# Performance work log

Measured on AMD Instinct MI355X. Metric: run time of the kernel, lower is better.

The kernel has to match this reference:

```python
import jax, jax.numpy as jnp
import numpy as np

N_NODES = 100000
N_EDGES = 600000
VOCAB = 50000
EMBED_DIM = 128
HIDDEN_DIM = 128


def gcn_conv(h, W, b, src, dst, n_nodes):
    """PyG GCNConv: x' = D^{-1/2} (A+I) D^{-1/2} X W + b.
    src/dst already include self-loops."""
    hw = h @ W                                   # [N, out]
    deg = jnp.zeros((n_nodes,), hw.dtype).at[dst].add(1.0)   # in-degree incl. self-loop
    dinv = jax.lax.rsqrt(deg)                    # deg >= 1 thanks to self-loops
    norm = dinv[src] * dinv[dst]                 # [E+N]
    msgs = norm[:, None] * hw[src]               # gather [E+N, out]
    out = jnp.zeros_like(hw).at[dst].add(msgs)   # scatter-aggregate
    return out + b


def setup_inputs() -> dict:
    key = jax.random.key(0)
    ks = jax.random.split(key, 8)
    x = jax.random.randint(ks[0], (N_NODES,), 0, VOCAB, dtype=jnp.int64 if jax.config.jax_enable_x64 else jnp.int32)
    edge_index = jax.random.randint(ks[1], (2, N_EDGES), 0, N_NODES, dtype=jnp.int32)
    emb = jax.random.normal(ks[2], (VOCAB, EMBED_DIM), dtype=jnp.float32)
    # Glorot-style scale for GCN weights
    W1 = jax.random.normal(ks[3], (EMBED_DIM, HIDDEN_DIM), dtype=jnp.float32) * (1.0 / np.sqrt(EMBED_DIM))
    b1 = jnp.zeros((HIDDEN_DIM,), dtype=jnp.float32)
    W2 = jax.random.normal(ks[4], (HIDDEN_DIM, HIDDEN_DIM), dtype=jnp.float32) * (1.0 / np.sqrt(HIDDEN_DIM))
    b2 = jnp.zeros((HIDDEN_DIM,), dtype=jnp.float32)
    return {"x": x, "edge_index": edge_index, "emb": emb, "W1": W1, "b1": b1, "W2": W2, "b2": b2}


def reference(x, edge_index, emb, W1, b1, W2, b2):
    n = x.shape[0]
    loops = jnp.arange(n, dtype=edge_index.dtype)
    src = jnp.concatenate([edge_index[0], loops])  # add self-loops once
    dst = jnp.concatenate([edge_index[1], loops])
    h = emb[x]                                     # [N, embed_dim] embedding lookup
    h = jax.nn.relu(gcn_conv(h, W1, b1, src, dst, n))
    h = jax.nn.relu(gcn_conv(h, W2, b2, src, dst, n))
    return h
```

## Files before the change

### kernel.cpp

```cpp
#include <hip/hip_runtime.h>


#define NDIM 128
#define PAD_K 136
#define SCAN_IPT 4
#define SCAN_BLK 256
#define SCAN_IPB (SCAN_BLK * SCAN_IPT)

typedef __bf16 bf16x8 __attribute__((ext_vector_type(8)));
typedef float f32x4 __attribute__((ext_vector_type(4)));

__device__ __forceinline__ float bf2f(unsigned short u) {
    union { unsigned int i; float f; } c;
    c.i = (unsigned int)u << 16;
    return c.f;
}
__device__ __forceinline__ unsigned short f2bf(float f) {
    __bf16 b = (__bf16)f;
    return __builtin_bit_cast(unsigned short, b);
}
__device__ __forceinline__ void unpack8(uint4 q, float* f) {
    f[0] = bf2f((unsigned short)(q.x & 0xffff));
    f[1] = bf2f((unsigned short)(q.x >> 16));
    f[2] = bf2f((unsigned short)(q.y & 0xffff));
    f[3] = bf2f((unsigned short)(q.y >> 16));
    f[4] = bf2f((unsigned short)(q.z & 0xffff));
    f[5] = bf2f((unsigned short)(q.z >> 16));
    f[6] = bf2f((unsigned short)(q.w & 0xffff));
    f[7] = bf2f((unsigned short)(q.w >> 16));
}

__global__ void degree_count(const int* __restrict__ dst, int* __restrict__ cnt, int E) {
    int e = blockIdx.x * blockDim.x + threadIdx.x;
    if (e < E) atomicAdd(&cnt[dst[e]], 1);
}

__global__ void scan_blocks(const int* __restrict__ in, int* __restrict__ out,
                            int* __restrict__ bsums, int n) {
    __shared__ int lds[SCAN_BLK];
    const int t = threadIdx.x;
    const int base = blockIdx.x * SCAN_IPB + t * SCAN_IPT;
    int v[SCAN_IPT];
    int s = 0;
#pragma unroll
    for (int k = 0; k < SCAN_IPT; ++k) { v[k] = (base + k < n) ? in[base + k] : 0; s += v[k]; }
    lds[t] = s;
    __syncthreads();
    for (int off = 1; off < SCAN_BLK; off <<= 1) {
        int x = (t >= off) ? lds[t - off] : 0;
        __syncthreads();
        lds[t] += x;
        __syncthreads();
    }
    if (t == SCAN_BLK - 1) bsums[blockIdx.x] = lds[t];
    int run = (t == 0) ? 0 : lds[t - 1];
#pragma unroll
    for (int k = 0; k < SCAN_IPT; ++k) {
        if (base + k < n) out[base + k] = run;
        run += v[k];
    }
}

__global__ void scan_partials(int* __restrict__ bsums, int nb) {
    __shared__ int lds[128];
    const int t = threadIdx.x;
    lds[t] = (t < nb) ? bsums[t] : 0;
    __syncthreads();
    for (int off = 1; off < 128; off <<= 1) {
        int x = (t >= off) ? lds[t - off] : 0;
        __syncthreads();
        lds[t] += x;
        __syncthreads();
    }
    if (t < nb) bsums[t] = (t == 0) ? 0 : lds[t - 1];
}

__global__ void add_offsets_dinv_wt(int* __restrict__ rp, const int* __restrict__ bsums,
                                    const int* __restrict__ cnt, float* __restrict__ dinv, int n,
                                    int nblkA,
                                    const float* __restrict__ W1, const float* __restrict__ W2,
                                    unsigned short* __restrict__ WT1,
                                    unsigned short* __restrict__ WT2) {
    if ((int)blockIdx.x < nblkA) {
        int i = blockIdx.x * blockDim.x + threadIdx.x;
        if (i < n) {
            rp[i] += bsums[i / SCAN_IPB];
            dinv[i] = rsqrtf((float)cnt[i] + 1.0f);
        }
    } else {
        int c = (blockIdx.x - nblkA) * blockDim.x + threadIdx.x;
        int cc = c & 16383;
        int j = cc >> 7, k = cc & 127;
        if (c < 16384) WT1[cc] = f2bf(W1[k * 128 + j]);
        else if (c < 32768) WT2[cc] = f2bf(W2[k * 128 + j]);
    }
}

__global__ void fill_edges(const int* __restrict__ src, const int* __restrict__ dst,
                           int* __restrict__ rp, const int* __restrict__ x,
                           const float* __restrict__ dinv, int4* __restrict__ ew, int E) {
    const int stride = gridDim.x * blockDim.x;
    int e = blockIdx.x * blockDim.x + threadIdx.x;
#pragma unroll
    for (int k = 0; k < 2; ++k, e += stride) {
        if (e < E) {
            int d = dst[e], s = src[e];
            int xs = x[s];
            float ds = dinv[s];
            int p = atomicAdd(&rp[d], 1);
            ew[p] = make_int4(s, xs, __float_as_int(ds), 0);
        }
    }
}

template <int MODE, bool SCALE>
__global__ __launch_bounds__(256, 4)
void gemm_mfma(const void* __restrict__ Asrc, const unsigned short* __restrict__ WTb,
               const float* __restrict__ dinv, unsigned short* __restrict__ outb, int n) {
    __shared__ __bf16 sBT[128 * PAD_K];
    const int tid = threadIdx.x;
    const int rbase = blockIdx.x * 64;

    {
        const uint4* bsrc = (const uint4*)WTb;
#pragma unroll
        for (int i = 0; i < 8; ++i) {
            int c = tid + i * 256;
            int j = c >> 4, u = c & 15;
            *(uint4*)&sBT[j * PAD_K + u * 8] = bsrc[c];
        }
    }
    __syncthreads();

    const int wave = tid >> 6, lane = tid & 63;
    const int quad = lane >> 4, lrow = lane & 15;
    int arow = rbase + wave * 16 + lrow;
    if (arow >= n) arow = n - 1;

    f32x4 acc[8];
#pragma unroll
    for (int nt = 0; nt < 8; ++nt) acc[nt] = (f32x4)0.0f;

#pragma unroll
    for (int ks = 0; ks < 4; ++ks) {
        const int kb = ks * 32 + quad * 8;
        bf16x8 a;
        if (MODE == 0) {
            const float4* A4 = (const float4*)Asrc;
            float4 v0 = A4[(size_t)arow * 32 + (kb >> 2)];
            float4 v1 = A4[(size_t)arow * 32 + (kb >> 2) + 1];
            a = (bf16x8){(__bf16)v0.x, (__bf16)v0.y, (__bf16)v0.z, (__bf16)v0.w,
                         (__bf16)v1.x, (__bf16)v1.y, (__bf16)v1.z, (__bf16)v1.w};
        } else {
            a = *(const bf16x8*)((const unsigned short*)Asrc + (size_t)arow * 128 + kb);
        }
#pragma unroll
        for (int nt = 0; nt < 8; ++nt) {
            bf16x8 b = *(const bf16x8*)&sBT[(nt * 16 + lrow) * PAD_K + kb];
            acc[nt] = __builtin_amdgcn_mfma_f32_16x16x32_bf16(a, b, acc[nt], 0, 0, 0);
        }
    }

#pragma unroll
    for (int r = 0; r < 4; ++r) {
        int grow = rbase + wave * 16 + quad * 4 + r;
        if (grow < n) {
            float dsc = SCALE ? dinv[grow] : 1.0f;
            unsigned short* orow = outb + (size_t)grow * NDIM + lrow;
#pragma unroll
            for (int nt = 0; nt < 8; ++nt)
                orow[nt * 16] = f2bf(SCALE ? dsc * acc[nt][r] : acc[nt][r]);
        }
    }
}

__global__ void aggregate1(const unsigned short* __restrict__ tab, const int* __restrict__ x,
                           const int* __restrict__ rp, const int4* __restrict__ ew,
                           const float* __restrict__ dinv, const float* __restrict__ bias,
                           unsigned short* __restrict__ outb, int n) {
    int t = blockIdx.x * blockDim.x + threadIdx.x;
    int i = t >> 4, u = t & 15;
    if (i >= n) return;
    const uint4* tab4 = (const uint4*)tab;
    float di = dinv[i];
    float acc[8];
    {
        float f[8];
        unpack8(tab4[(size_t)x[i] * 16 + u], f);
#pragma unroll
        for (int k = 0; k < 8; ++k) acc[k] = di * f[k];
    }
    int j = (i == 0) ? 0 : rp[i - 1];
    const int end = rp[i];
    for (; j + 4 <= end; j += 4) {
        int4 e0 = ew[j], e1 = ew[j + 1], e2 = ew[j + 2], e3 = ew[j + 3];
        uint4 q0 = tab4[(size_t)e0.y * 16 + u];
        uint4 q1 = tab4[(size_t)e1.y * 16 + u];
        uint4 q2 = tab4[(size_t)e2.y * 16 + u];
        uint4 q3 = tab4[(size_t)e3.y * 16 + u];
        float f0[8], f1[8], f2[8], f3[8];
        unpack8(q0, f0); unpack8(q1, f1); unpack8(q2, f2); unpack8(q3, f3);
        float n0 = __int_as_float(e0.z), n1 = __int_as_float(e1.z);
        float n2 = __int_as_float(e2.z), n3 = __int_as_float(e3.z);
#pragma unroll
        for (int k = 0; k < 8; ++k) {
            float s01 = fmaf(n0, f0[k], n1 * f1[k]);
            float s23 = fmaf(n2, f2[k], n3 * f3[k]);
            acc[k] += s01 + s23;
        }
    }
    for (; j < end; ++j) {
        int4 e = ew[j];
        uint4 q = tab4[(size_t)e.y * 16 + u];
        float f[8];
        unpack8(q, f);
        float nm = __int_as_float(e.z);
#pragma unroll
        for (int k = 0; k < 8; ++k) acc[k] = fmaf(nm, f[k], acc[k]);
    }
    const float4 b0 = ((const float4*)bias)[u * 2];
    const float4 b1 = ((const float4*)bias)[u * 2 + 1];
    float r[8];
    r[0] = fmaxf(fmaf(di, acc[0], b0.x), 0.0f);
    r[1] = fmaxf(fmaf(di, acc[1], b0.y), 0.0f);
    r[2] = fmaxf(fmaf(di, acc[2], b0.z), 0.0f);
    r[3] = fmaxf(fmaf(di, acc[3], b0.w), 0.0f);
    r[4] = fmaxf(fmaf(di, acc[4], b1.x), 0.0f);
    r[5] = fmaxf(fmaf(di, acc[5], b1.y), 0.0f);
    r[6] = fmaxf(fmaf(di, acc[6], b1.z), 0.0f);
    r[7] = fmaxf(fmaf(di, acc[7], b1.w), 0.0f);
    uint4 o;
    o.x = (unsigned)f2bf(r[0]) | ((unsigned)f2bf(r[1]) << 16);
    o.y = (unsigned)f2bf(r[2]) | ((unsigned)f2bf(r[3]) << 16);
    o.z = (unsigned)f2bf(r[4]) | ((unsigned)f2bf(r[5]) << 16);
    o.w = (unsigned)f2bf(r[6]) | ((unsigned)f2bf(r[7]) << 16);
    ((uint4*)outb)[(size_t)i * 16 + u] = o;
}

__global__ void aggregate2(const unsigned short* __restrict__ vs, const int* __restrict__ rp,
                           const int4* __restrict__ ew, const float* __restrict__ dinv,
                           const float* __restrict__ bias, float* __restrict__ out, int n) {
    int t = blockIdx.x * blockDim.x + threadIdx.x;
    int i = t >> 4, u = t & 15;
    if (i >= n) return;
    const uint4* vs4 = (const uint4*)vs;
    float acc[8];
    unpack8(vs4[(size_t)i * 16 + u], acc);
    int j = (i == 0) ? 0 : rp[i - 1];
    const int end = rp[i];
    for (; j + 4 <= end; j += 4) {
        int s0 = ew[j].x, s1 = ew[j + 1].x, s2 = ew[j + 2].x, s3 = ew[j + 3].x;
        uint4 q0 = vs4[(size_t)s0 * 16 + u];
        uint4 q1 = vs4[(size_t)s1 * 16 + u];
        uint4 q2 = vs4[(size_t)s2 * 16 + u];
        uint4 q3 = vs4[(size_t)s3 * 16 + u];
        float f0[8], f1[8], f2[8], f3[8];
        unpack8(q0, f0); unpack8(q1, f1); unpack8(q2, f2); unpack8(q3, f3);
#pragma unroll
        for (int k = 0; k < 8; ++k) acc[k] += (f0[k] + f1[k]) + (f2[k] + f3[k]);
    }
    for (; j < end; ++j) {
        int s = ew[j].x;
        uint4 q = vs4[(size_t)s * 16 + u];
        float f[8];
        unpack8(q, f);
#pragma unroll
        for (int k = 0; k < 8; ++k) acc[k] += f[k];
    }
    float di = dinv[i];
    const float4 b0 = ((const float4*)bias)[u * 2];
    const float4 b1 = ((const float4*)bias)[u * 2 + 1];
    float4 r0, r1;
    r0.x = fmaxf(fmaf(di, acc[0], b0.x), 0.0f);
    r0.y = fmaxf(fmaf(di, acc[1], b0.y), 0.0f);
    r0.z = fmaxf(fmaf(di, acc[2], b0.z), 0.0f);
    r0.w = fmaxf(fmaf(di, acc[3], b0.w), 0.0f);
    r1.x = fmaxf(fmaf(di, acc[4], b1.x), 0.0f);
    r1.y = fmaxf(fmaf(di, acc[5], b1.y), 0.0f);
    r1.z = fmaxf(fmaf(di, acc[6], b1.z), 0.0f);
    r1.w = fmaxf(fmaf(di, acc[7], b1.w), 0.0f);
    ((float4*)out)[(size_t)i * 32 + u * 2] = r0;
    ((float4*)out)[(size_t)i * 32 + u * 2 + 1] = r1;
}

extern "C" void kernel_launch(void* const* d_in, const int* in_sizes, int n_in,
                              void* d_out, int out_size, void* d_ws, size_t ws_size,
                              hipStream_t stream) {
    const int* x = (const int*)d_in[0];
    const int* edge_index = (const int*)d_in[1];
    const float* emb = (const float*)d_in[2];
    const float* W1 = (const float*)d_in[3];
    const float* b1 = (const float*)d_in[4];
    const float* W2 = (const float*)d_in[5];
    const float* b2 = (const float*)d_in[6];
    float* out = (float*)d_out;

    const int N = in_sizes[0];
    const int E = in_sizes[1] / 2;
    const int V = in_sizes[2] / NDIM;
    const int* src = edge_index;
    const int* dst = edge_index + E;

    char* p = (char*)d_ws;
    auto alloc = [&](size_t bytes) {
        char* q = p;
        p += (bytes + 511) & ~(size_t)511;
        return q;
    };
    int* cnt = (int*)alloc((size_t)N * sizeof(int));
    int* rp = (int*)alloc((size_t)N * sizeof(int));
    float* dinv = (float*)alloc((size_t)N * sizeof(float));
    int* bsums = (int*)alloc(128 * sizeof(int));
    int4* ew = (int4*)alloc((size_t)E * sizeof(int4));
    unsigned short* WT1 = (unsigned short*)alloc(16384 * sizeof(unsigned short));
    unsigned short* WT2 = (unsigned short*)alloc(16384 * sizeof(unsigned short));
    unsigned short* embW1 = (unsigned short*)alloc((size_t)V * NDIM * sizeof(unsigned short));
    unsigned short* h1b = (unsigned short*)alloc((size_t)N * NDIM * sizeof(unsigned short));
    unsigned short* vs2 = (unsigned short*)alloc((size_t)N * NDIM * sizeof(unsigned short));
    (void)ws_size;

    const int NB = (N + SCAN_IPB - 1) / SCAN_IPB;
    const int nblkA = (N + 255) / 256;

    hipMemsetAsync(cnt, 0, (size_t)N * sizeof(int), stream);
    degree_count<<<(E + 255) / 256, 256, 0, stream>>>(dst, cnt, E);
    scan_blocks<<<NB, SCAN_BLK, 0, stream>>>(cnt, rp, bsums, N);
    scan_partials<<<1, 128, 0, stream>>>(bsums, NB);
    add_offsets_dinv_wt<<<nblkA + 128, 256, 0, stream>>>(rp, bsums, cnt, dinv, N, nblkA,
                                                         W1, W2, WT1, WT2);
    fill_edges<<<(E / 2 + 255) / 256, 256, 0, stream>>>(src, dst, rp, x, dinv, ew, E);

    const int agg_blocks = (int)(((size_t)N * 16 + 255) / 256);

    gemm_mfma<0, false><<<(V + 63) / 64, 256, 0, stream>>>(emb, WT1, nullptr, embW1, V);
    aggregate1<<<agg_blocks, 256, 0, stream>>>(embW1, x, rp, ew, dinv, b1, h1b, N);
    gemm_mfma<1, true><<<(N + 63) / 64, 256, 0, stream>>>(h1b, WT2, dinv, vs2, N);
    aggregate2<<<agg_blocks, 256, 0, stream>>>(vs2, rp, ew, dinv, b2, out, N);
}
```

Measured before the change: 242.2 us.

## Compress edge records to int2 and process two nodes per aggregation thread group

Edge records shrink from 16 to 8 bytes by packing the vocab index (16 bits) and an fp16 source normalisation into one word. Each 16-lane group in both aggregation kernels now handles two nodes, interleaving their gathers to raise memory-level parallelism. Degree counting and edge filling process four edges per thread with loads batched ahead of the atomics. The packing assumes vocab ids fit in 16 bits and accepts fp16 precision for the norm factor; halving the thread count may lower occupancy and worsen load imbalance.

```diff
diff --git a/kernel.cpp b/kernel.cpp
--- a/kernel.cpp
+++ b/kernel.cpp
@@ -1,4 +1,5 @@
 #include <hip/hip_runtime.h>
+#include <hip/hip_fp16.h>
 
 
 #define NDIM 128
@@ -18,6 +19,13 @@
 __device__ __forceinline__ unsigned short f2bf(float f) {
     __bf16 b = (__bf16)f;
     return __builtin_bit_cast(unsigned short, b);
+}
+__device__ __forceinline__ unsigned short f2h(float f) {
+    __half h = __float2half_rn(f);
+    return __builtin_bit_cast(unsigned short, h);
+}
+__device__ __forceinline__ float h2f(unsigned short u) {
+    return __half2float(__builtin_bit_cast(__half, u));
 }
 __device__ __forceinline__ void unpack8(uint4 q, float* f) {
     f[0] = bf2f((unsigned short)(q.x & 0xffff));
@@ -31,8 +39,13 @@
 }
 
 __global__ void degree_count(const int* __restrict__ dst, int* __restrict__ cnt, int E) {
+    const int stride = gridDim.x * blockDim.x;
     int e = blockIdx.x * blockDim.x + threadIdx.x;
-    if (e < E) atomicAdd(&cnt[dst[e]], 1);
+#pragma unroll
+    for (int k = 0; k < 4; ++k) {
+        int ee = e + k * stride;
+        if (ee < E) atomicAdd(&cnt[dst[ee]], 1);
+    }
 }
 
 __global__ void scan_blocks(const int* __restrict__ in, int* __restrict__ out,
@@ -98,17 +111,26 @@
 
 __global__ void fill_edges(const int* __restrict__ src, const int* __restrict__ dst,
                            int* __restrict__ rp, const int* __restrict__ x,
-                           const float* __restrict__ dinv, int4* __restrict__ ew, int E) {
+                           const float* __restrict__ dinv, int2* __restrict__ ew, int E) {
     const int stride = gridDim.x * blockDim.x;
-    int e = blockIdx.x * blockDim.x + threadIdx.x;
-#pragma unroll
-    for (int k = 0; k < 2; ++k, e += stride) {
-        if (e < E) {
-            int d = dst[e], s = src[e];
-            int xs = x[s];
-            float ds = dinv[s];
-            int p = atomicAdd(&rp[d], 1);
-            ew[p] = make_int4(s, xs, __float_as_int(ds), 0);
+    const int e0 = blockIdx.x * blockDim.x + threadIdx.x;
+    int s[4], d[4];
+#pragma unroll
+    for (int k = 0; k < 4; ++k) {
+        int ee = e0 + k * stride;
+        if (ee < E) { s[k] = src[ee]; d[k] = dst[ee]; } else { s[k] = -1; }
+    }
+    int xs[4];
+    float ds[4];
+#pragma unroll
+    for (int k = 0; k < 4; ++k) {
+        if (s[k] >= 0) { xs[k] = x[s[k]]; ds[k] = dinv[s[k]]; }
+    }
+#pragma unroll
+    for (int k = 0; k < 4; ++k) {
+        if (s[k] >= 0) {
+            int p = atomicAdd(&rp[d[k]], 1);
+            ew[p] = make_int2(s[k], (int)(((unsigned)f2h(ds[k]) << 16) | (unsigned)xs[k]));
         }
     }
 }
@@ -175,112 +197,229 @@
 }
 
 __global__ void aggregate1(const unsigned short* __restrict__ tab, const int* __restrict__ x,
-                           const int* __restrict__ rp, const int4* __restrict__ ew,
+                           const int* __restrict__ rp, const int2* __restrict__ ew,
                            const float* __restrict__ dinv, const float* __restrict__ bias,
-                           unsigned short* __restrict__ outb, int n) {
+                           unsigned short* __restrict__ outb, int n, int half) {
     int t = blockIdx.x * blockDim.x + threadIdx.x;
-    int i = t >> 4, u = t & 15;
-    if (i >= n) return;
+    int g = t >> 4, u = t & 15;
+    if (g >= half) return;
     const uint4* tab4 = (const uint4*)tab;
-    float di = dinv[i];
-    float acc[8];
+    const int i0 = g, i1 = g + half;
+    const bool has1 = (i1 < n);
+    float di0 = dinv[i0];
+    float di1 = has1 ? dinv[i1] : 0.0f;
+    float acc0[8], acc1[8];
     {
         float f[8];
-        unpack8(tab4[(size_t)x[i] * 16 + u], f);
-#pragma unroll
-        for (int k = 0; k < 8; ++k) acc[k] = di * f[k];
-    }
-    int j = (i == 0) ? 0 : rp[i - 1];
-    const int end = rp[i];
-    for (; j + 4 <= end; j += 4) {
-        int4 e0 = ew[j], e1 = ew[j + 1], e2 = ew[j + 2], e3 = ew[j + 3];
-        uint4 q0 = tab4[(size_t)e0.y * 16 + u];
-        uint4 q1 = tab4[(size_t)e1.y * 16 + u];
-        uint4 q2 = tab4[(size_t)e2.y * 16 + u];
-        uint4 q3 = tab4[(size_t)e3.y * 16 + u];
-        float f0[8], f1[8], f2[8], f3[8];
-        unpack8(q0, f0); unpack8(q1, f1); unpack8(q2, f2); unpack8(q3, f3);
-        float n0 = __int_as_float(e0.z), n1 = __int_as_float(e1.z);
-        float n2 = __int_as_float(e2.z), n3 = __int_as_float(e3.z);
+        unpack8(tab4[(size_t)x[i0] * 16 + u], f);
+#pragma unroll
+        for (int k = 0; k < 8; ++k) acc0[k] = di0 * f[k];
+    }
+    if (has1) {
+        float f[8];
+        unpack8(tab4[(size_t)x[i1] * 16 + u], f);
+#pragma unroll
+        for (int k = 0; k < 8; ++k) acc1[k] = di1 * f[k];
+    }
+    int j0 = (i0 == 0) ? 0 : rp[i0 - 1];
+    const int e0 = rp[i0];
+    int j1 = has1 ? rp[i1 - 1] : 0;
+    const int e1 = has1 ? rp[i1] : 0;
+
+    while (j0 + 2 <= e0 && j1 + 2 <= e1) {
+        int2 a0 = ew[j0], a1 = ew[j0 + 1], c0 = ew[j1], c1 = ew[j1 + 1];
+        uint4 qa0 = tab4[(size_t)(a0.y & 0xffff) * 16 + u];
+        uint4 qa1 = tab4[(size_t)(a1.y & 0xffff) * 16 + u];
+        uint4 qc0 = tab4[(size_t)(c0.y & 0xffff) * 16 + u];
+        uint4 qc1 = tab4[(size_t)(c1.y & 0xffff) * 16 + u];
+        float fa0[8], fa1[8], fc0[8], fc1[8];
+        unpack8(qa0, fa0); unpack8(qa1, fa1); unpack8(qc0, fc0); unpack8(qc1, fc1);
+        float na0 = h2f((unsigned short)((unsigned)a0.y >> 16));
+        float na1 = h2f((unsigned short)((unsigned)a1.y >> 16));
+        float nc0 = h2f((unsigned short)((unsigned)c0.y >> 16));
+        float nc1 = h2f((unsigned short)((unsigned)c1.y >> 16));
 #pragma unroll
         for (int k = 0; k < 8; ++k) {
-            float s01 = fmaf(n0, f0[k], n1 * f1[k]);
-            float s23 = fmaf(n2, f2[k], n3 * f3[k]);
-            acc[k] += s01 + s23;
-        }
-    }
-    for (; j < end; ++j) {
-        int4 e = ew[j];
-        uint4 q = tab4[(size_t)e.y * 16 + u];
+            acc0[k] += fmaf(na0, fa0[k], na1 * fa1[k]);
+            acc1[k] += fmaf(nc0, fc0[k], nc1 * fc1[k]);
+        }
+        j0 += 2; j1 += 2;
+    }
+    for (; j0 + 2 <= e0; j0 += 2) {
+        int2 a0 = ew[j0], a1 = ew[j0 + 1];
+        uint4 qa0 = tab4[(size_t)(a0.y & 0xffff) * 16 + u];
+        uint4 qa1 = tab4[(size_t)(a1.y & 0xffff) * 16 + u];
+        float fa0[8], fa1[8];
+        unpack8(qa0, fa0); unpack8(qa1, fa1);
+        float na0 = h2f((unsigned short)((unsigned)a0.y >> 16));
+        float na1 = h2f((unsigned short)((unsigned)a1.y >> 16));
+#pragma unroll
+        for (int k = 0; k < 8; ++k) acc0[k] += fmaf(na0, fa0[k], na1 * fa1[k]);
+    }
+    if (j0 < e0) {
+        int2 a = ew[j0];
+        uint4 q = tab4[(size_t)(a.y & 0xffff) * 16 + u];
         float f[8];
         unpack8(q, f);
-        float nm = __int_as_float(e.z);
-#pragma unroll
-        for (int k = 0; k < 8; ++k) acc[k] = fmaf(nm, f[k], acc[k]);
-    }
+        float nm = h2f((unsigned short)((unsigned)a.y >> 16));
+#pragma unroll
+        for (int k = 0; k < 8; ++k) acc0[k] = fmaf(nm, f[k], acc0[k]);
+    }
+    for (; j1 + 2 <= e1; j1 += 2) {
+        int2 c0 = ew[j1], c1 = ew[j1 + 1];
+        uint4 qc0 = tab4[(size_t)(c0.y & 0xffff) * 16 + u];
+        uint4 qc1 = tab4[(size_t)(c1.y & 0xffff) * 16 + u];
+        float fc0[8], fc1[8];
+        unpack8(qc0, fc0); unpack8(qc1, fc1);
+        float nc0 = h2f((unsigned short)((unsigned)c0.y >> 16));
+        float nc1 = h2f((unsigned short)((unsigned)c1.y >> 16));
+#pragma unroll
+        for (int k = 0; k < 8; ++k) acc1[k] += fmaf(nc0, fc0[k], nc1 * fc1[k]);
+    }
+    if (j1 < e1) {
+        int2 c = ew[j1];
+        uint4 q = tab4[(size_t)(c.y & 0xffff) * 16 + u];
+        float f[8];
+        unpack8(q, f);
+        float nm = h2f((unsigned short)((unsigned)c.y >> 16));
+#pragma unroll
+        for (int k = 0; k < 8; ++k) acc1[k] = fmaf(nm, f[k], acc1[k]);
+    }
+
     const float4 b0 = ((const float4*)bias)[u * 2];
     const float4 b1 = ((const float4*)bias)[u * 2 + 1];
-    float r[8];
-    r[0] = fmaxf(fmaf(di, acc[0], b0.x), 0.0f);
-    r[1] = fmaxf(fmaf(di, acc[1], b0.y), 0.0f);
-    r[2] = fmaxf(fmaf(di, acc[2], b0.z), 0.0f);
-    r[3] = fmaxf(fmaf(di, acc[3], b0.w), 0.0f);
-    r[4] = fmaxf(fmaf(di, acc[4], b1.x), 0.0f);
-    r[5] = fmaxf(fmaf(di, acc[5], b1.y), 0.0f);
-    r[6] = fmaxf(fmaf(di, acc[6], b1.z), 0.0f);
-    r[7] = fmaxf(fmaf(di, acc[7], b1.w), 0.0f);
-    uint4 o;
-    o.x = (unsigned)f2bf(r[0]) | ((unsigned)f2bf(r[1]) << 16);
-    o.y = (unsigned)f2bf(r[2]) | ((unsigned)f2bf(r[3]) << 16);
-    o.z = (unsigned)f2bf(r[4]) | ((unsigned)f2bf(r[5]) << 16);
-    o.w = (unsigned)f2bf(r[6]) | ((unsigned)f2bf(r[7]) << 16);
-    ((uint4*)outb)[(size_t)i * 16 + u] = o;
+    {
+        float r[8];
+        r[0] = fmaxf(fmaf(di0, acc0[0], b0.x), 0.0f);
+        r[1] = fmaxf(fmaf(di0, acc0[1], b0.y), 0.0f);
+        r[2] = fmaxf(fmaf(di0, acc0[2], b0.z), 0.0f);
+        r[3] = fmaxf(fmaf(di0, acc0[3], b0.w), 0.0f);
+        r[4] = fmaxf(fmaf(di0, acc0[4], b1.x), 0.0f);
+        r[5] = fmaxf(fmaf(di0, acc0[5], b1.y), 0.0f);
+        r[6] = fmaxf(fmaf(di0, acc0[6], b1.z), 0.0f);
+        r[7] = fmaxf(fmaf(di0, acc0[7], b1.w), 0.0f);
+        uint4 o;
+        o.x = (unsigned)f2bf(r[0]) | ((unsigned)f2bf(r[1]) << 16);
+        o.y = (unsigned)f2bf(r[2]) | ((unsigned)f2bf(r[3]) << 16);
+        o.z = (unsigned)f2bf(r[4]) | ((unsigned)f2bf(r[5]) << 16);
+        o.w = (unsigned)f2bf(r[6]) | ((unsigned)f2bf(r[7]) << 16);
+        ((uint4*)outb)[(size_t)i0 * 16 + u] = o;
+    }
+    if (has1) {
+        float r[8];
+        r[0] = fmaxf(fmaf(di1, acc1[0], b0.x), 0.0f);
+        r[1] = fmaxf(fmaf(di1, acc1[1], b0.y), 0.0f);
+        r[2] = fmaxf(fmaf(di1, acc1[2], b0.z), 0.0f);
+        r[3] = fmaxf(fmaf(di1, acc1[3], b0.w), 0.0f);
+        r[4] = fmaxf(fmaf(di1, acc1[4], b1.x), 0.0f);
+        r[5] = fmaxf(fmaf(di1, acc1[5], b1.y), 0.0f);
+        r[6] = fmaxf(fmaf(di1, acc1[6], b1.z), 0.0f);
+        r[7] = fmaxf(fmaf(di1, acc1[7], b1.w), 0.0f);
+        uint4 o;
+        o.x = (unsigned)f2bf(r[0]) | ((unsigned)f2bf(r[1]) << 16);
+        o.y = (unsigned)f2bf(r[2]) | ((unsigned)f2bf(r[3]) << 16);
+        o.z = (unsigned)f2bf(r[4]) | ((unsigned)f2bf(r[5]) << 16);
+        o.w = (unsigned)f2bf(r[6]) | ((unsigned)f2bf(r[7]) << 16);
+        ((uint4*)outb)[(size_t)i1 * 16 + u] = o;
+    }
 }
 
 __global__ void aggregate2(const unsigned short* __restrict__ vs, const int* __restrict__ rp,
-                           const int4* __restrict__ ew, const float* __restrict__ dinv,
-                           const float* __restrict__ bias, float* __restrict__ out, int n) {
+                           const int2* __restrict__ ew, const float* __restrict__ dinv,
+                           const float* __restrict__ bias, float* __restrict__ out,
+                           int n, int half) {
     int t = blockIdx.x * blockDim.x + threadIdx.x;
-    int i = t >> 4, u = t & 15;
-    if (i >= n) return;
+    int g = t >> 4, u = t & 15;
+    if (g >= half) return;
     const uint4* vs4 = (const uint4*)vs;
-    float acc[8];
-    unpack8(vs4[(size_t)i * 16 + u], acc);
-    int j = (i == 0) ? 0 : rp[i - 1];
-    const int end = rp[i];
-    for (; j + 4 <= end; j += 4) {
-        int s0 = ew[j].x, s1 = ew[j + 1].x, s2 = ew[j + 2].x, s3 = ew[j + 3].x;
-        uint4 q0 = vs4[(size_t)s0 * 16 + u];
-        uint4 q1 = vs4[(size_t)s1 * 16 + u];
-        uint4 q2 = vs4[(size_t)s2 * 16 + u];
-        uint4 q3 = vs4[(size_t)s3 * 16 + u];
-        float f0[8], f1[8], f2[8], f3[8];
-        unpack8(q0, f0); unpack8(q1, f1); unpack8(q2, f2); unpack8(q3, f3);
-#pragma unroll
-        for (int k = 0; k < 8; ++k) acc[k] += (f0[k] + f1[k]) + (f2[k] + f3[k]);
-    }
-    for (; j < end; ++j) {
-        int s = ew[j].x;
-        uint4 q = vs4[(size_t)s * 16 + u];
+    const int i0 = g, i1 = g + half;
+    const bool has1 = (i1 < n);
+    float acc0[8], acc1[8];
+    unpack8(vs4[(size_t)i0 * 16 + u], acc0);
+    if (has1) unpack8(vs4[(size_t)i1 * 16 + u], acc1);
+    int j0 = (i0 == 0) ? 0 : rp[i0 - 1];
+    const int e0 = rp[i0];
+    int j1 = has1 ? rp[i1 - 1] : 0;
+    const int e1 = has1 ? rp[i1] : 0;
+
+    while (j0 + 2 <= e0 && j1 + 2 <= e1) {
+        int s00 = ew[j0].x, s01 = ew[j0 + 1].x, s10 = ew[j1].x, s11 = ew[j1 + 1].x;
+        uint4 q00 = vs4[(size_t)s00 * 16 + u];
+        uint4 q01 = vs4[(size_t)s01 * 16 + u];
+        uint4 q10 = vs4[(size_t)s10 * 16 + u];
+        uint4 q11 = vs4[(size_t)s11 * 16 + u];
+        float f00[8], f01[8], f10[8], f11[8];
+        unpack8(q00, f00); unpack8(q01, f01); unpack8(q10, f10); unpack8(q11, f11);
+#pragma unroll
+        for (int k = 0; k < 8; ++k) {
+            acc0[k] += f00[k] + f01[k];
+            acc1[k] += f10[k] + f11[k];
+        }
+        j0 += 2; j1 += 2;
+    }
+    for (; j0 + 2 <= e0; j0 += 2) {
+        int s00 = ew[j0].x, s01 = ew[j0 + 1].x;
+        uint4 q00 = vs4[(size_t)s00 * 16 + u];
+        uint4 q01 = vs4[(size_t)s01 * 16 + u];
+        float f00[8], f01[8];
+        unpack8(q00, f00); unpack8(q01, f01);
+#pragma unroll
+        for (int k = 0; k < 8; ++k) acc0[k] += f00[k] + f01[k];
+    }
+    if (j0 < e0) {
+        uint4 q = vs4[(size_t)ew[j0].x * 16 + u];
         float f[8];
         unpack8(q, f);
 #pragma unroll
-        for (int k = 0; k < 8; ++k) acc[k] += f[k];
-    }
-    float di = dinv[i];
+        for (int k = 0; k < 8; ++k) acc0[k] += f[k];
+    }
+    for (; j1 + 2 <= e1; j1 += 2) {
+        int s10 = ew[j1].x, s11 = ew[j1 + 1].x;
+        uint4 q10 = vs4[(size_t)s10 * 16 + u];
+        uint4 q11 = vs4[(size_t)s11 * 16 + u];
+        float f10[8], f11[8];
+        unpack8(q10, f10); unpack8(q11, f11);
+#pragma unroll
+        for (int k = 0; k < 8; ++k) acc1[k] += f10[k] + f11[k];
+    }
+    if (j1 < e1) {
+        uint4 q = vs4[(size_t)ew[j1].x * 16 + u];
+        float f[8];
+        unpack8(q, f);
+#pragma unroll
+        for (int k = 0; k < 8; ++k) acc1[k] += f[k];
+    }
+
     const float4 b0 = ((const float4*)bias)[u * 2];
     const float4 b1 = ((const float4*)bias)[u * 2 + 1];
-    float4 r0, r1;
-    r0.x = fmaxf(fmaf(di, acc[0], b0.x), 0.0f);
-    r0.y = fmaxf(fmaf(di, acc[1], b0.y), 0.0f);
-    r0.z = fmaxf(fmaf(di, acc[2], b0.z), 0.0f);
-    r0.w = fmaxf(fmaf(di, acc[3], b0.w), 0.0f);
-    r1.x = fmaxf(fmaf(di, acc[4], b1.x), 0.0f);
-    r1.y = fmaxf(fmaf(di, acc[5], b1.y), 0.0f);
-    r1.z = fmaxf(fmaf(di, acc[6], b1.z), 0.0f);
-    r1.w = fmaxf(fmaf(di, acc[7], b1.w), 0.0f);
-    ((float4*)out)[(size_t)i * 32 + u * 2] = r0;
-    ((float4*)out)[(size_t)i * 32 + u * 2 + 1] = r1;
+    {
+        float di = dinv[i0];
+        float4 r0, r1;
+        r0.x = fmaxf(fmaf(di, acc0[0], b0.x), 0.0f);
+        r0.y = fmaxf(fmaf(di, acc0[1], b0.y), 0.0f);
+        r0.z = fmaxf(fmaf(di, acc0[2], b0.z), 0.0f);
+        r0.w = fmaxf(fmaf(di, acc0[3], b0.w), 0.0f);
+        r1.x = fmaxf(fmaf(di, acc0[4], b1.x), 0.0f);
+        r1.y = fmaxf(fmaf(di, acc0[5], b1.y), 0.0f);
+        r1.z = fmaxf(fmaf(di, acc0[6], b1.z), 0.0f);
+        r1.w = fmaxf(fmaf(di, acc0[7], b1.w), 0.0f);
+        ((float4*)out)[(size_t)i0 * 32 + u * 2] = r0;
+        ((float4*)out)[(size_t)i0 * 32 + u * 2 + 1] = r1;
+    }
+    if (has1) {
+        float di = dinv[i1];
+        float4 r0, r1;
+        r0.x = fmaxf(fmaf(di, acc1[0], b0.x), 0.0f);
+        r0.y = fmaxf(fmaf(di, acc1[1], b0.y), 0.0f);
+        r0.z = fmaxf(fmaf(di, acc1[2], b0.z), 0.0f);
+        r0.w = fmaxf(fmaf(di, acc1[3], b0.w), 0.0f);
+        r1.x = fmaxf(fmaf(di, acc1[4], b1.x), 0.0f);
+        r1.y = fmaxf(fmaf(di, acc1[5], b1.y), 0.0f);
+        r1.z = fmaxf(fmaf(di, acc1[6], b1.z), 0.0f);
+        r1.w = fmaxf(fmaf(di, acc1[7], b1.w), 0.0f);
+        ((float4*)out)[(size_t)i1 * 32 + u * 2] = r0;
+        ((float4*)out)[(size_t)i1 * 32 + u * 2 + 1] = r1;
+    }
 }
 
 extern "C" void kernel_launch(void* const* d_in, const int* in_sizes, int n_in,
@@ -311,7 +450,7 @@
     int* rp = (int*)alloc((size_t)N * sizeof(int));
     float* dinv = (float*)alloc((size_t)N * sizeof(float));
     int* bsums = (int*)alloc(128 * sizeof(int));
-    int4* ew = (int4*)alloc((size_t)E * sizeof(int4));
+    int2* ew = (int2*)alloc((size_t)E * sizeof(int2));
     unsigned short* WT1 = (unsigned short*)alloc(16384 * sizeof(unsigned short));
     unsigned short* WT2 = (unsigned short*)alloc(16384 * sizeof(unsigned short));
     unsigned short* embW1 = (unsigned short*)alloc((size_t)V * NDIM * sizeof(unsigned short));
@@ -321,19 +460,20 @@
 
     const int NB = (N + SCAN_IPB - 1) / SCAN_IPB;
     const int nblkA = (N + 255) / 256;
+    const int half = (N + 1) / 2;
 
     hipMemsetAsync(cnt, 0, (size_t)N * sizeof(int), stream);
-    degree_count<<<(E + 255) / 256, 256, 0, stream>>>(dst, cnt, E);
+    degree_count<<<(E / 4 + 255) / 256, 256, 0, stream>>>(dst, cnt, E);
     scan_blocks<<<NB, SCAN_BLK, 0, stream>>>(cnt, rp, bsums, N);
     scan_partials<<<1, 128, 0, stream>>>(bsums, NB);
     add_offsets_dinv_wt<<<nblkA + 128, 256, 0, stream>>>(rp, bsums, cnt, dinv, N, nblkA,
                                                          W1, W2, WT1, WT2);
-    fill_edges<<<(E / 2 + 255) / 256, 256, 0, stream>>>(src, dst, rp, x, dinv, ew, E);
-
-    const int agg_blocks = (int)(((size_t)N * 16 + 255) / 256);
+    fill_edges<<<(E / 4 + 255) / 256, 256, 0, stream>>>(src, dst, rp, x, dinv, ew, E);
+
+    const int agg_blocks = (int)(((size_t)half * 16 + 255) / 256);
 
     gemm_mfma<0, false><<<(V + 63) / 64, 256, 0, stream>>>(emb, WT1, nullptr, embW1, V);
-    aggregate1<<<agg_blocks, 256, 0, stream>>>(embW1, x, rp, ew, dinv, b1, h1b, N);
+    aggregate1<<<agg_blocks, 256, 0, stream>>>(embW1, x, rp, ew, dinv, b1, h1b, N, half);
     gemm_mfma<1, true><<<(N + 63) / 64, 256, 0, stream>>>(h1b, WT2, dinv, vs2, N);
-    aggregate2<<<agg_blocks, 256, 0, stream>>>(vs2, rp, ew, dinv, b2, out, N);
-}
+    aggregate2<<<agg_blocks, 256, 0, stream>>>(vs2, rp, ew, dinv, b2, out, N, half);
+}
```

Result: slower. 251.8 us (+4.0%).
